# Performance work log

Measured on AMD Instinct MI355X. Metric: run time of the kernel, lower is better.

## Reference

```python
import jax, jax.numpy as jnp
import numpy as np
from jax import lax

B, T, HID, NH = 4, 2048, 1024, 16
D = HID // NH
LN_EPS = 1e-5
NORM_EPS = 1e-6


def setup_inputs() -> dict:
    key = jax.random.key(0)
    ks = jax.random.split(key, 3)
    s = 0.02
    return {
        "x": jax.random.normal(ks[0], (B, T, HID), jnp.float32),
        "ln_g": jnp.ones((HID,), jnp.float32),
        "ln_b": jnp.zeros((HID,), jnp.float32),
        "w_qkvb": jax.random.normal(ks[1], (HID, 4 * HID), jnp.float32) * s,
        "b_qkvb": jnp.zeros((4 * HID,), jnp.float32),
        "w_out": jax.random.normal(ks[2], (HID, HID), jnp.float32) * s,
        "b_out": jnp.zeros((HID,), jnp.float32),
    }


def reference(x, ln_g, ln_b, w_qkvb, b_qkvb, w_out, b_out):
    b, t = x.shape[:2]
    # LayerNorm (biased variance, eps=1e-5, matching nn.LayerNorm)
    mu = jnp.mean(x, axis=-1, keepdims=True)
    var = jnp.mean((x - mu) ** 2, axis=-1, keepdims=True)
    normed = (x - mu) * lax.rsqrt(var + LN_EPS) * ln_g + ln_b

    proj = normed @ w_qkvb + b_qkvb  # [B,T,4H]
    q, k, v, beta_pre = jnp.split(proj, 4, axis=-1)
    beta = jax.nn.sigmoid(beta_pre)

    def heads(a):  # [B,T,H] -> [T,B,NH,D] (time-major for scan)
        return a.reshape(b, t, NH, D).transpose(1, 0, 2, 3)

    q, k, v, beta = heads(q), heads(k), heads(v), heads(beta)
    # F.normalize(k, dim=-1, eps=1e-6)
    k = k / jnp.maximum(jnp.linalg.norm(k, axis=-1, keepdims=True), NORM_EPS)

    S0 = jnp.zeros((b, NH, D, D), x.dtype)

    def step(S, inp):
        q_t, k_t, v_t, beta_t = inp  # each [B,NH,D]
        retrieval = jnp.einsum('bhij,bhj->bhi', S, k_t)
        S = S + jnp.einsum('bhi,bhj->bhij', beta_t * (v_t - retrieval), k_t)
        o_t = jnp.einsum('bhij,bhj->bhi', S, q_t)
        return S, o_t

    _, out_t = lax.scan(step, S0, (q, k, v, beta))  # out_t: [T,B,NH,D]
    scan_out = out_t.transpose(1, 0, 2, 3).reshape(b, t, NH * D)
    return x + scan_out @ w_out + b_out
```

## Files before the change

### kernel.cpp

```cpp
#include <hip/hip_runtime.h>
#include <hip/hip_bf16.h>

typedef __attribute__((ext_vector_type(8))) short short8;
typedef __attribute__((ext_vector_type(4))) float f32x4;

#define P72 72

__device__ __forceinline__ unsigned short f2bf(float f) {
    union { float f; unsigned int u; } v; v.f = f;
    unsigned int r = (v.u + 0x7FFFu + ((v.u >> 16) & 1u)) >> 16;
    return (unsigned short)r;
}
__device__ __forceinline__ float bf2f(unsigned short b) {
    union { unsigned int u; float f; } v; v.u = ((unsigned int)b) << 16; return v.f;
}

#define WAVE_SYNC() do { __asm__ volatile("s_waitcnt lgkmcnt(0)" ::: "memory"); \
                         __builtin_amdgcn_sched_barrier(0); } while (0)

#define LGKM_BARRIER() do { __asm__ volatile("s_waitcnt lgkmcnt(0)" ::: "memory"); \
                            __builtin_amdgcn_s_barrier(); \
                            __builtin_amdgcn_sched_barrier(0); } while (0)

#define ASYNC16(G, L) __builtin_amdgcn_global_load_lds( \
// ... 134 lines not shown
#pragma unroll
                for (int m = 0; m < 4; m++)
#pragma unroll
                    for (int n = 0; n < 4; n++)
#pragma unroll
                        for (int j = 0; j < 4; j++) {
                            float val = acc[m][n][j] + bias_r[n];
                            if (sec == 3) val = 1.0f / (1.0f + expf(-val));
                            SMEM[(m * 16 + kg * 4 + j) * 136 + wc * 64 + n * 16 + r15] = f2bf(val);
                        }
            }
            __syncthreads();
            const int tl = tid >> 2, sg = tid & 3;
            const int gm = M0 + p * 64 + tl;
            const int b = gm >> 11, t = gm & 2047;
            const int h = hA + (sg >> 1), d0 = (sg & 1) * 32;
            const int colbase = sg * 32;
            const size_t dst = ((size_t)(b * 16 + h) * 2048 + t) * 64 + d0;
#pragma unroll
            for (int i = 0; i < 4; i++) {
                uint4 v = *(const uint4*)&SMEM[tl * 136 + colbase + i * 8];
                *(uint4*)(arr + dst + i * 8) = v;
            }
        }
    } else {
        float* stf = (float*)SMEM;
#pragma unroll
        for (int p = 0; p < 4; ++p) {
            __syncthreads();
            if (wr == (p >> 1)) {
#pragma unroll
                for (int mm = 0; mm < 2; mm++)
#pragma unroll
                    for (int n = 0; n < 4; n++)
#pragma unroll
                        for (int j = 0; j < 4; j++)
                            stf[(mm * 16 + kg * 4 + j) * 132 + wc * 64 + n * 16 + r15] =
                                acc[(p & 1) * 2 + mm][n][j] + bias_r[n];
            }
            __syncthreads();
            const int rl = tid >> 3, sg = (tid & 7) * 16;
            const size_t rowo = (size_t)(M0 + p * 32 + rl) * N + N0 + sg;
#pragma unroll
            for (int i = 0; i < 4; i++) {
                float4 v = *(const float4*)&stf[rl * 132 + sg + i * 4];
                float4 r = *(const float4*)(resid + rowo + i * 4);
                v.x += r.x; v.y += r.y; v.z += r.z; v.w += r.w;
                *(float4*)(outf + rowo + i * 4) = v;
            }
        }
    }
}

__global__ __launch_bounds__(512, 2) void gemm256(
    const unsigned short* __restrict__ A, const unsigned short* __restrict__ Bt,
    const float* __restrict__ bias, int K, int n0_off,
    unsigned short* __restrict__ qo, unsigned short* __restrict__ ko,
    unsigned short* __restrict__ vo, unsigned short* __restrict__ bo)
{
    __shared__ __align__(16) unsigned short SMEM[73728];
    const int tid = threadIdx.x;
    const int nwg = (int)(gridDim.x * gridDim.y);
    const int flat = (int)(blockIdx.y * gridDim.x + blockIdx.x);
    const int id2 = (flat & 7) * (nwg >> 3) + (flat >> 3);
    const int M0 = (id2 / (int)gridDim.x) * 256;
    const int N0 = (id2 % (int)gridDim.x) * 128 + n0_off;

    const int lane = tid & 63, wv = tid >> 6;
    const int wr = wv >> 2, wc = wv & 3;
    const int r15 = lane & 15, kg = lane >> 4;
    const int swz = r15 & 7;

    const int srow = lane >> 3;
    const int schk = (lane & 7) ^ srow;
    const unsigned short* Asrc = A  + (size_t)(M0 + wv * 8 + srow) * K + schk * 8;
    const unsigned short* Bsrc = Bt + (size_t)(N0 + wv * 8 + srow) * K + schk * 8;

    float bias_r[2];
    bias_r[0] = bias[N0 + wc * 32 + r15];
    bias_r[1] = bias[N0 + wc * 32 + 16 + r15];
    __builtin_amdgcn_sched_barrier(0);

    auto stageA = [&](int b_, int ko_, int i_) {
        ASYNC16(Asrc + (size_t)i_ * 64 * K + ko_,
                &SMEM[b_ * 24576 + (i_ * 64 + wv * 8) * 64]);
    };
    auto stageB = [&](int b_, int ko_, int i_) {
        ASYNC16(Bsrc + (size_t)i_ * 64 * K + ko_,
                &SMEM[b_ * 24576 + 16384 + (i_ * 64 + wv * 8) * 64]);
    };

#pragma unroll
    for (int i = 0; i < 4; i++) stageA(0, 0, i);
    stageB(0, 0, 0); stageB(0, 0, 1);
#pragma unroll
    for (int i = 0; i < 4; i++) stageA(1, 64, i);
    stageB(1, 64, 0); stageB(1, 64, 1);

    f32x4 acc[8][2] = {};

#define PH_PRE() do { __builtin_amdgcn_s_barrier(); \
                      __asm__ volatile("s_waitcnt lgkmcnt(0)" ::: "memory"); \
                      __builtin_amdgcn_sched_barrier(0); \
                      __builtin_amdgcn_s_setprio(1); } while (0)
#define PH_POST() do { __builtin_amdgcn_s_setprio(0); \
                       __builtin_amdgcn_sched_barrier(0); \
                       __builtin_amdgcn_s_barrier(); } while (0)

    const int NT = K >> 6;
    int cur = 0;
    for (int t = 0; t < NT; ++t) {
        if (t + 1 < NT) { __asm__ volatile("s_waitcnt vmcnt(6)" ::: "memory"); }
        else            { __asm__ volatile("s_waitcnt vmcnt(0)" ::: "memory"); }
        __builtin_amdgcn_s_barrier();
        __builtin_amdgcn_sched_barrier(0);

        const unsigned short* Ab = &SMEM[cur * 24576];
        const unsigned short* Bb = &SMEM[cur * 24576 + 16384];
        int nb = cur + 2; if (nb >= 3) nb -= 3;
        const int nko = (t + 2) * 64;
        const bool pf = (t + 2 < NT);

        short8 af[4], bf[2];
#pragma unroll
        for (int m = 0; m < 4; m++)
            af[m] = *(const short8*)&Ab[(wr * 128 + m * 16 + r15) * 64 + (kg ^ swz) * 8];
#pragma unroll
        for (int n = 0; n < 2; n++)
            bf[n] = *(const short8*)&Bb[(wc * 32 + n * 16 + r15) * 64 + (kg ^ swz) * 8];
        if (pf) { stageA(nb, nko, 0); stageA(nb, nko, 1); }
        PH_PRE();
#pragma unroll
        for (int m = 0; m < 4; m++)
#pragma unroll
            for (int n = 0; n < 2; n++)
                acc[m][n] = __builtin_amdgcn_mfma_f32_16x16x32_bf16(af[m], bf[n], acc[m][n], 0, 0, 0);
        PH_POST();
#pragma unroll
        for (int m = 0; m < 4; m++)
            af[m] = *(const short8*)&Ab[(wr * 128 + (m + 4) * 16 + r15) * 64 + (kg ^ swz) * 8];
        if (pf) { stageA(nb, nko, 2); stageA(nb, nko, 3); }
        PH_PRE();
#pragma unroll
        for (int m = 0; m < 4; m++)
#pragma unroll
            for (int n = 0; n < 2; n++)
                acc[m + 4][n] = __builtin_amdgcn_mfma_f32_16x16x32_bf16(af[m], bf[n], acc[m + 4][n], 0, 0, 0);
        PH_POST();
#pragma unroll
        for (int m = 0; m < 4; m++)
            af[m] = *(const short8*)&Ab[(wr * 128 + m * 16 + r15) * 64 + ((4 + kg) ^ swz) * 8];
#pragma unroll
        for (int n = 0; n < 2; n++)
            bf[n] = *(const short8*)&Bb[(wc * 32 + n * 16 + r15) * 64 + ((4 + kg) ^ swz) * 8];
        if (pf) { stageB(nb, nko, 0); stageB(nb, nko, 1); }
        PH_PRE();
#pragma unroll
        for (int m = 0; m < 4; m++)
#pragma unroll
            for (int n = 0; n < 2; n++)
                acc[m][n] = __builtin_amdgcn_mfma_f32_16x16x32_bf16(af[m], bf[n], acc[m][n], 0, 0, 0);
        PH_POST();
#pragma unroll
        for (int m = 0; m < 4; m++)
            af[m] = *(const short8*)&Ab[(wr * 128 + (m + 4) * 16 + r15) * 64 + ((4 + kg) ^ swz) * 8];
        PH_PRE();
#pragma unroll
        for (int m = 0; m < 4; m++)
#pragma unroll
            for (int n = 0; n < 2; n++)
                acc[m + 4][n] = __builtin_amdgcn_mfma_f32_16x16x32_bf16(af[m], bf[n], acc[m + 4][n], 0, 0, 0);
        __builtin_amdgcn_s_setprio(0);
        __builtin_amdgcn_sched_barrier(0);

        cur += 1; if (cur >= 3) cur = 0;
    }
#undef PH_PRE
#undef PH_POST

    const int sec = N0 >> 10;
    const int hA = (N0 & 1023) >> 6;
    unsigned short* arr = (sec == 0) ? qo : (sec == 1) ? ko : (sec == 2) ? vo : bo;
#pragma unroll
    for (int p = 0; p < 2; ++p) {
        __syncthreads();
        if (wr == p) {
#pragma unroll
            for (int m = 0; m < 8; m++)
#pragma unroll
                for (int n = 0; n < 2; n++)
#pragma unroll
                    for (int j = 0; j < 4; j++) {
                        float val = acc[m][n][j] + bias_r[n];
                        if (sec == 3) val = 1.0f / (1.0f + expf(-val));
                        SMEM[(m * 16 + kg * 4 + j) * 136 + wc * 32 + n * 16 + r15] = f2bf(val);
                    }
        }
        __syncthreads();
        const int row = tid >> 2, sg = tid & 3;
        const int gm = M0 + p * 128 + row;
        const int b = gm >> 11, tt = gm & 2047;
        const int h = hA + (sg >> 1), d0 = (sg & 1) * 32;
        const size_t dst = ((size_t)(b * 16 + h) * 2048 + tt) * 64 + d0;
#pragma unroll
        for (int i = 0; i < 4; i++) {
            uint4 v = *(const uint4*)&SMEM[row * 136 + sg * 32 + i * 8];
            *(uint4*)(arr + dst + i * 8) = v;
        }
    }
}

__global__ __launch_bounds__(256) void prep_kernel(
    const unsigned short* __restrict__ Kpre, const unsigned short* __restrict__ Vin,
    const unsigned short* __restrict__ Bin,
    unsigned short* __restrict__ Kb, unsigned short* __restrict__ A0g,
    float* __restrict__ A0Dg, unsigned short* __restrict__ KTg,
    unsigned short* __restrict__ VTg, unsigned short* __restrict__ BTg)
{
    __shared__ __align__(16) unsigned short Ks[64 * P72];
    __shared__ __align__(16) unsigned short Vs[64 * P72];
    __shared__ __align__(16) unsigned short Bs[64 * P72];
    __shared__ __align__(16) unsigned short Os[64 * P72];
    const int cid = blockIdx.x, tid = threadIdx.x;
    const size_t gbase = (size_t)cid * 4096;
    const int r0 = tid >> 2, c0 = (tid & 3) * 16;
    {
        uint4 k0 = *(const uint4*)(Kpre + gbase + r0 * 64 + c0), k1 = *(const uint4*)(Kpre + gbase + r0 * 64 + c0 + 8);
        uint4 v0 = *(const uint4*)(Vin + gbase + r0 * 64 + c0),  v1 = *(const uint4*)(Vin + gbase + r0 * 64 + c0 + 8);
        uint4 b0 = *(const uint4*)(Bin + gbase + r0 * 64 + c0),  b1 = *(const uint4*)(Bin + gbase + r0 * 64 + c0 + 8);
        *(uint4*)&Ks[r0 * P72 + c0] = k0; *(uint4*)&Ks[r0 * P72 + c0 + 8] = k1;
        *(uint4*)&Vs[r0 * P72 + c0] = v0; *(uint4*)&Vs[r0 * P72 + c0 + 8] = v1;
        *(uint4*)&Bs[r0 * P72 + c0] = b0; *(uint4*)&Bs[r0 * P72 + c0 + 8] = b1;
    }
    __syncthreads();
    {
        const int row = tid >> 2, seg = tid & 3;
        float v[16]; float ss = 0.f;
#pragma unroll
        for (int q = 0; q < 16; q++) { v[q] = bf2f(Ks[row * P72 + seg * 16 + q]); ss = fmaf(v[q], v[q], ss); }
        ss += __shfl_xor(ss, 1); ss += __shfl_xor(ss, 2);
        const float inv = 1.0f / fmaxf(sqrtf(ss), 1e-6f);
        unsigned short t16[16];
#pragma unroll
        for (int q = 0; q < 16; q++) t16[q] = f2bf(v[q] * inv);
        *(uint4*)&Ks[row * P72 + seg * 16]     = *(uint4*)&t16[0];
        *(uint4*)&Ks[row * P72 + seg * 16 + 8] = *(uint4*)&t16[8];
        *(uint4*)(Kb + gbase + row * 64 + seg * 16)     = *(uint4*)&t16[0];
        *(uint4*)(Kb + gbase + row * 64 + seg * 16 + 8) = *(uint4*)&t16[8];
    }
    __syncthreads();
    const int lane = tid & 63, w = tid >> 6;
    const int r15 = lane & 15, kg = lane >> 4;
    f32x4 acc[4] = {{0,0,0,0},{0,0,0,0},{0,0,0,0},{0,0,0,0}};
#pragma unroll
    for (int ks = 0; ks < 2; ks++) {
        short8 afr = *(const short8*)&Ks[(w * 16 + r15) * P72 + ks * 32 + kg * 8];
#pragma unroll
        for (int n = 0; n < 4; n++) {
            short8 bfr = *(const short8*)&Ks[(n * 16 + r15) * P72 + ks * 32 + kg * 8];
            acc[n] = __builtin_amdgcn_mfma_f32_16x16x32_bf16(afr, bfr, acc[n], 0, 0, 0);
        }
    }
#pragma unroll
    for (int n = 0; n < 4; n++) {
#pragma unroll
        for (int j = 0; j < 4; j++) {
            const int s = w * 16 + kg * 4 + j, r = n * 16 + r15;
            Os[s * P72 + r] = (r < s) ? f2bf(acc[n][j]) : (unsigned short)0;
        }
        if (n == w) {
            float4 d;
            d.x = (r15 < kg * 4 + 0) ? acc[n][0] : 0.f;
            d.y = (r15 < kg * 4 + 1) ? acc[n][1] : 0.f;
            d.z = (r15 < kg * 4 + 2) ? acc[n][2] : 0.f;
            d.w = (r15 < kg * 4 + 3) ? acc[n][3] : 0.f;
            *(float4*)(A0Dg + (size_t)cid * 1024 + w * 256 + r15 * 16 + kg * 4) = d;
        }
    }
    __syncthreads();
    {
        uint4 x0 = *(const uint4*)&Os[r0 * P72 + c0];
        uint4 x1 = *(const uint4*)&Os[r0 * P72 + c0 + 8];
        *(uint4*)(A0g + gbase + r0 * 64 + c0) = x0;
        *(uint4*)(A0g + gbase + r0 * 64 + c0 + 8) = x1;
    }
    {
        const int d = tid >> 2, s0 = (tid & 3) * 16;
        unsigned short tk[16], tv[16], tb[16];
#pragma unroll
        for (int k = 0; k < 16; k++) {
            tk[k] = Ks[(s0 + k) * P72 + d];
            tv[k] = Vs[(s0 + k) * P72 + d];
            tb[k] = Bs[(s0 + k) * P72 + d];
        }
        *(uint4*)(KTg + gbase + (size_t)d * 64 + s0)     = *(uint4*)&tk[0];
        *(uint4*)(KTg + gbase + (size_t)d * 64 + s0 + 8) = *(uint4*)&tk[8];
        *(uint4*)(VTg + gbase + (size_t)d * 64 + s0)     = *(uint4*)&tv[0];
        *(uint4*)(VTg + gbase + (size_t)d * 64 + s0 + 8) = *(uint4*)&tv[8];
        *(uint4*)(BTg + gbase + (size_t)d * 64 + s0)     = *(uint4*)&tb[0];
        *(uint4*)(BTg + gbase + (size_t)d * 64 + s0 + 8) = *(uint4*)&tb[8];
    }
}

__global__ __launch_bounds__(256, 1) void fused_scan_kernel(
    const unsigned short* __restrict__ A0g, const unsigned short* __restrict__ Kb,
    const unsigned short* __restrict__ KTg, const float* __restrict__ A0Dg,
    const unsigned short* __restrict__ VTg, const unsigned short* __restrict__ BTg,
    unsigned short* __restrict__ Scg, unsigned short* __restrict__ UTg,
    const unsigned short* __restrict__ NORM, const unsigned short* __restrict__ WQT,
    const float* __restrict__ bias, unsigned short* __restrict__ qo,
    const float* __restrict__ w_out, unsigned short* __restrict__ WOT)
{
    __shared__ __align__(16) unsigned char POOL[120832];
    unsigned short* us = (unsigned short*)POOL;
    const int tid = threadIdx.x;

    if (blockIdx.x < 64) {
        unsigned short* sK  = us;
        unsigned short* sKT = us + 9216;
        unsigned short* sA0 = us + 18432;
        unsigned short* sVT = us + 27648;
        unsigned short* sBT = us + 36864;
        float* sA0D = (float*)(POOL + 92160);
        unsigned short* Sbf = us + 51200;
        unsigned short* UTs = us + 55808;

        const int bh = blockIdx.x;
        const int lane = tid & 63, w = tid >> 6;
        const int r15 = lane & 15, kg = lane >> 4;
        const int sr = tid >> 2, sc = (tid & 3) * 16;
        const int qr = 16 * w + (lane >> 2), qc = (lane & 3) * 16;
        const size_t base0 = (size_t)bh * 32 * 4096;
        const size_t baseD = (size_t)bh * 32 * 1024;
        const int dOff = (w * 16 + (sr & 15)) * 20 + (tid & 3) * 4;

        f32x4 Sreg[4] = {};
        uint4 g[10]; float4 gD;

        const uint4 z4 = {0u, 0u, 0u, 0u};
        *(uint4*)&Sbf[sr * P72 + sc] = z4;
        *(uint4*)&Sbf[sr * P72 + sc + 8] = z4;
        {
            const size_t gb = base0 + sr * 64 + sc;
            g[0] = *(const uint4*)(Kb  + gb); g[1] = *(const uint4*)(Kb  + gb + 8);
            g[2] = *(const uint4*)(KTg + gb); g[3] = *(const uint4*)(KTg + gb + 8);
            g[4] = *(const uint4*)(A0g + gb); g[5] = *(const uint4*)(A0g + gb + 8);
            g[6] = *(const uint4*)(VTg + gb); g[7] = *(const uint4*)(VTg + gb + 8);
            g[8] = *(const uint4*)(BTg + gb); g[9] = *(const uint4*)(BTg + gb + 8);
            gD   = *(const float4*)(A0Dg + baseD + tid * 4);
            *(uint4*)&sK [sr * P72 + sc] = g[0]; *(uint4*)&sK [sr * P72 + sc + 8] = g[1];
            *(uint4*)&sKT[sr * P72 + sc] = g[2]; *(uint4*)&sKT[sr * P72 + sc + 8] = g[3];
            *(uint4*)&sA0[sr * P72 + sc] = g[4]; *(uint4*)&sA0[sr * P72 + sc + 8] = g[5];
            *(uint4*)&sVT[sr * P72 + sc] = g[6]; *(uint4*)&sVT[sr * P72 + sc + 8] = g[7];
            *(uint4*)&sBT[sr * P72 + sc] = g[8]; *(uint4*)&sBT[sr * P72 + sc + 8] = g[9];
            *(float4*)&sA0D[dOff] = gD;
        }

#pragma unroll 1
        for (int c = 0; c < 32; ++c) {
            const int cur = c & 1, nxt = cur ^ 1;
            LGKM_BARRIER();
            if (c < 31) {
                const size_t gb = base0 + (size_t)(c + 1) * 4096 + sr * 64 + sc;
                g[0] = *(const uint4*)(Kb  + gb); g[1] = *(const uint4*)(Kb  + gb + 8);
                g[2] = *(const uint4*)(KTg + gb); g[3] = *(const uint4*)(KTg + gb + 8);
                g[4] = *(const uint4*)(A0g + gb); g[5] = *(const uint4*)(A0g + gb + 8);
                g[6] = *(const uint4*)(VTg + gb); g[7] = *(const uint4*)(VTg + gb + 8);
                g[8] = *(const uint4*)(BTg + gb); g[9] = *(const uint4*)(BTg + gb + 8);
                gD   = *(const float4*)(A0Dg + baseD + (size_t)(c + 1) * 1024 + tid * 4);
            }
            const unsigned short* KsC  = &sK [cur * 4608];
            const unsigned short* KTsC = &sKT[cur * 4608];
            const unsigned short* A0C  = &sA0[cur * 4608];
            const unsigned short* VTC  = &sVT[cur * 4608];
            const unsigned short* BTC  = &sBT[cur * 4608];
            const float*          A0DC = &sA0D[cur * 1280];

            *(uint4*)&UTs[(16 * w + r15) * P72 + kg * 16] = z4;
            *(uint4*)&UTs[(16 * w + r15) * P72 + kg * 16 + 8] = z4;

            {
                uint4 a = *(const uint4*)&Sbf[qr * P72 + qc];
                uint4 b2 = *(const uint4*)&Sbf[qr * P72 + qc + 8];
                const unsigned FL = 0x80008000u;
                a.x ^= FL; a.y ^= FL; a.z ^= FL; a.w ^= FL;
                b2.x ^= FL; b2.y ^= FL; b2.z ^= FL; b2.w ^= FL;
                const size_t so = base0 + (size_t)c * 4096 + qr * 64 + qc;
                *(uint4*)(Scg + so) = a;
                *(uint4*)(Scg + so + 8) = b2;
            }

            f32x4 y[4];
#pragma unroll
            for (int st = 0; st < 4; st++) {
                ushort4 vv = *(const ushort4*)&VTC[(16 * w + r15) * P72 + st * 16 + kg * 4];
                y[st][0] = bf2f(vv.x); y[st][1] = bf2f(vv.y);
                y[st][2] = bf2f(vv.z); y[st][3] = bf2f(vv.w);
            }
#pragma unroll
            for (int ks = 0; ks < 2; ks++) {
                short8 bfr = *(const short8*)&Sbf[(16 * w + r15) * P72 + ks * 32 + kg * 8];
#pragma unroll
                for (int st = 0; st < 4; st++) {
                    short8 afr = *(const short8*)&KsC[(st * 16 + r15) * P72 + ks * 32 + kg * 8];
                    y[st] = __builtin_amdgcn_mfma_f32_16x16x32_bf16(afr, bfr, y[st], 0, 0, 0);
                }
            }

#pragma unroll
            for (int b = 0; b < 4; b++) {
                if (b > 0) {
                    WAVE_SYNC();
                    f32x4 corr = {};
                    {
                        short8 afr = *(const short8*)&A0C[(b * 16 + r15) * P72 + kg * 8];
                        short8 bfr = *(const short8*)&UTs[(16 * w + r15) * P72 + kg * 8];
                        corr = __builtin_amdgcn_mfma_f32_16x16x32_bf16(afr, bfr, corr, 0, 0, 0);
                    }
                    if (b == 3) {
                        short8 afr = *(const short8*)&A0C[(b * 16 + r15) * P72 + 32 + kg * 8];
                        short8 bfr = *(const short8*)&UTs[(16 * w + r15) * P72 + 32 + kg * 8];
                        corr = __builtin_amdgcn_mfma_f32_16x16x32_bf16(afr, bfr, corr, 0, 0, 0);
                    }
                    y[b] = y[b] - corr;
                }
                ushort4 bt4 = *(const ushort4*)&BTC[(16 * w + r15) * P72 + b * 16 + kg * 4];
                const float bta0 = bf2f(bt4.x), bta1 = bf2f(bt4.y);
                const float bta2 = bf2f(bt4.z), bta3 = bf2f(bt4.w);
                float us0 = 0.f, us1 = 0.f, us2 = 0.f, us3 = 0.f;
#pragma unroll
                for (int own = 0; own < 4; own++) {
                    const f32x4 c40 = *(const f32x4*)&A0DC[(b * 16 + own * 4 + 0) * 20 + kg * 4];
                    const f32x4 c41 = *(const f32x4*)&A0DC[(b * 16 + own * 4 + 1) * 20 + kg * 4];
                    const f32x4 c42 = *(const f32x4*)&A0DC[(b * 16 + own * 4 + 2) * 20 + kg * 4];
                    const f32x4 c43 = *(const f32x4*)&A0DC[(b * 16 + own * 4 + 3) * 20 + kg * 4];
                    if (kg == own) {
                        us0 = bta0 * y[b][0];
                        us1 = bta1 * (y[b][1] - c40[1] * us0);
                        us2 = bta2 * (y[b][2] - c40[2] * us0 - c41[2] * us1);
                        us3 = bta3 * (y[b][3] - c40[3] * us0 - c41[3] * us1 - c42[3] * us2);
                    }
                    const int src = own * 16 + r15;
                    const float u0 = __shfl(us0, src), u1 = __shfl(us1, src);
                    const float u2 = __shfl(us2, src), u3 = __shfl(us3, src);
                    if (kg > own)
                        y[b] = y[b] - (c40 * u0 + c41 * u1 + c42 * u2 + c43 * u3);
                }
                ushort4 up;
                up.x = f2bf(us0); up.y = f2bf(us1); up.z = f2bf(us2); up.w = f2bf(us3);
                *(ushort4*)&UTs[(16 * w + r15) * P72 + b * 16 + kg * 4] = up;
            }
            WAVE_SYNC();

            {
                uint4 a = *(const uint4*)&UTs[qr * P72 + qc];
                uint4 b2 = *(const uint4*)&UTs[qr * P72 + qc + 8];
                const size_t so = base0 + (size_t)c * 4096 + qr * 64 + qc;
                *(uint4*)(UTg + so) = a;
                *(uint4*)(UTg + so + 8) = b2;
            }

#pragma unroll
            for (int ks = 0; ks < 2; ks++) {
                short8 afr = *(const short8*)&UTs[(16 * w + r15) * P72 + ks * 32 + kg * 8];
#pragma unroll
                for (int n = 0; n < 4; n++) {
                    short8 bfr = *(const short8*)&KTsC[(n * 16 + r15) * P72 + ks * 32 + kg * 8];
                    Sreg[n] = __builtin_amdgcn_mfma_f32_16x16x32_bf16(afr, bfr, Sreg[n], 0, 0, 0);
                }
            }
#pragma unroll
            for (int n = 0; n < 4; n++)
#pragma unroll
                for (int jj = 0; jj < 4; jj++)
                    Sbf[(16 * w + kg * 4 + jj) * P72 + n * 16 + r15] = f2bf(-Sreg[n][jj]);

            if (c < 31) {
                *(uint4*)&sK [nxt * 4608 + sr * P72 + sc] = g[0]; *(uint4*)&sK [nxt * 4608 + sr * P72 + sc + 8] = g[1];
                *(uint4*)&sKT[nxt * 4608 + sr * P72 + sc] = g[2]; *(uint4*)&sKT[nxt * 4608 + sr * P72 + sc + 8] = g[3];
                *(uint4*)&sA0[nxt * 4608 + sr * P72 + sc] = g[4]; *(uint4*)&sA0[nxt * 4608 + sr * P72 + sc + 8] = g[5];
                *(uint4*)&sVT[nxt * 4608 + sr * P72 + sc] = g[6]; *(uint4*)&sVT[nxt * 4608 + sr * P72 + sc + 8] = g[7];
                *(uint4*)&sBT[nxt * 4608 + sr * P72 + sc] = g[8]; *(uint4*)&sBT[nxt * 4608 + sr * P72 + sc + 8] = g[9];
                *(float4*)&sA0D[nxt * 1280 + dOff] = gD;
            }
        }
    } else if (blockIdx.x < 64 + 512) {
        unsigned short* SMEM = us;
        const int blk = blockIdx.x - 64;
        const int M0 = (blk >> 3) * 128, N0 = (blk & 7) * 128;
        const int K = 1024;
        const int lane = tid & 63;
        const int w = tid >> 6, wr = w >> 1, wc = w & 1;
        const int r15 = lane & 15, kg = lane >> 4;
        const int lr = lane >> 2, lc = (lane & 3) * 8;

        const unsigned short* Arow0 = NORM + (size_t)(M0 + w * 16 + lr) * K + lc;
        const unsigned short* Arow1 = NORM + (size_t)(M0 + 64 + w * 16 + lr) * K + lc;
        const unsigned short* Brow0 = WQT + (size_t)(N0 + w * 16 + lr) * K + lc;
        const unsigned short* Brow1 = WQT + (size_t)(N0 + 64 + w * 16 + lr) * K + lc;

        f32x4 acc[4][4] = {};

        ASYNC16(Arow0, &SMEM[(w * 16) * 32]);
        ASYNC16(Arow1, &SMEM[(64 + w * 16) * 32]);
        ASYNC16(Brow0, &SMEM[8192 + (w * 16) * 32]);
        ASYNC16(Brow1, &SMEM[8192 + (64 + w * 16) * 32]);

        int cur = 0;
        for (int k0 = 0; k0 < K; k0 += 32) {
            if (k0 + 32 < K) {
                const int nb = (cur ^ 1) * 4096;
                ASYNC16(Arow0 + k0 + 32, &SMEM[nb + (w * 16) * 32]);
                ASYNC16(Arow1 + k0 + 32, &SMEM[nb + (64 + w * 16) * 32]);
                ASYNC16(Brow0 + k0 + 32, &SMEM[8192 + nb + (w * 16) * 32]);
                ASYNC16(Brow1 + k0 + 32, &SMEM[8192 + nb + (64 + w * 16) * 32]);
                __asm__ volatile("s_waitcnt vmcnt(4)" ::: "memory");
            } else {
                __asm__ volatile("s_waitcnt vmcnt(0)" ::: "memory");
            }
            __builtin_amdgcn_s_barrier();
            __builtin_amdgcn_sched_barrier(0);
            const int cb = cur * 4096;
            short8 af[4], bf[4];
#pragma unroll
            for (int m = 0; m < 4; m++)
                af[m] = *(const short8*)&SMEM[cb + (wr * 64 + m * 16 + r15) * 32 + kg * 8];
#pragma unroll
            for (int n = 0; n < 4; n++)
                bf[n] = *(const short8*)&SMEM[8192 + cb + (wc * 64 + n * 16 + r15) * 32 + kg * 8];
#pragma unroll
            for (int m = 0; m < 4; m++)
#pragma unroll
                for (int n = 0; n < 4; n++)
                    acc[m][n] = __builtin_amdgcn_mfma_f32_16x16x32_bf16(af[m], bf[n], acc[m][n], 0, 0, 0);
            __builtin_amdgcn_sched_barrier(0);
            __builtin_amdgcn_s_barrier();
            cur ^= 1;
        }

        float bias_r[4];
#pragma unroll
        for (int n = 0; n < 4; n++) bias_r[n] = bias[N0 + wc * 64 + n * 16 + r15];
        const int hA = N0 >> 6;
#pragma unroll
        for (int p = 0; p < 2; ++p) {
            __syncthreads();
            if (wr == p) {
#pragma unroll
                for (int m = 0; m < 4; m++)
#pragma unroll
                    for (int n = 0; n < 4; n++)
#pragma unroll
                        for (int j = 0; j < 4; j++)
                            SMEM[(m * 16 + kg * 4 + j) * 136 + wc * 64 + n * 16 + r15] =
                                f2bf(acc[m][n][j] + bias_r[n]);
            }
            __syncthreads();
            const int tl = tid >> 2, sg = tid & 3;
            const int gm = M0 + p * 64 + tl;
            const int b = gm >> 11, t = gm & 2047;
            const int h = hA + (sg >> 1), d0 = (sg & 1) * 32;
            const int colbase = sg * 32;
            const size_t dst = ((size_t)(b * 16 + h) * 2048 + t) * 64 + d0;
#pragma unroll
            for (int i = 0; i < 4; i++) {
                uint4 v = *(const uint4*)&SMEM[tl * 136 + colbase + i * 8];
                *(uint4*)(qo + dst + i * 8) = v;
            }
        }
    } else {
        float* tile = (float*)POOL;
        const int blk = blockIdx.x - 64 - 512;
        const int c0 = (blk & 31) * 32, r0 = (blk >> 5) * 32;
        const int tx = tid & 31, ty = tid >> 5;
#pragma unroll
        for (int yy = 0; yy < 32; yy += 8)
            tile[(ty + yy) * 33 + tx] = w_out[(size_t)(r0 + ty + yy) * 1024 + c0 + tx];
        __syncthreads();
#pragma unroll
        for (int yy = 0; yy < 32; yy += 8)
            WOT[(size_t)(c0 + ty + yy) * 1024 + r0 + tx] = f2bf(tile[tx * 33 + ty + yy]);
    }
}

__global__ __launch_bounds__(256) void out_kernel(
    const unsigned short* __restrict__ Qb, const unsigned short* __restrict__ Kb,
    const unsigned short* __restrict__ Scg, const unsigned short* __restrict__ UTg,
    unsigned short* __restrict__ attn)
{
    __shared__ __align__(16) unsigned short Qs[64 * P72];
    __shared__ __align__(16) unsigned short Kbs[64 * P72];
    __shared__ __align__(16) unsigned short Scs[64 * P72];
    __shared__ __align__(16) unsigned short UTss[64 * P72];
    __shared__ __align__(16) unsigned short Ms[64 * P72];
    __shared__ __align__(16) unsigned short Osb[64 * P72];
    const int blk = blockIdx.x, tid = threadIdx.x;
    const int bh = blk >> 5, cc = blk & 31;
    const size_t gbase = (size_t)blk * 4096;
    const int lane = tid & 63, w = tid >> 6;
    const int r15 = lane & 15, kg = lane >> 4;
    {
        const int r0 = tid >> 2, c0 = (tid & 3) * 16;
        uint4 q0 = *(const uint4*)(Qb + gbase + r0 * 64 + c0),  q1 = *(const uint4*)(Qb + gbase + r0 * 64 + c0 + 8);
        uint4 k0 = *(const uint4*)(Kb + gbase + r0 * 64 + c0),  k1 = *(const uint4*)(Kb + gbase + r0 * 64 + c0 + 8);
        uint4 s0 = *(const uint4*)(Scg + gbase + r0 * 64 + c0), s1 = *(const uint4*)(Scg + gbase + r0 * 64 + c0 + 8);
        uint4 u0 = *(const uint4*)(UTg + gbase + r0 * 64 + c0), u1 = *(const uint4*)(UTg + gbase + r0 * 64 + c0 + 8);
        *(uint4*)&Qs [r0 * P72 + c0] = q0; *(uint4*)&Qs [r0 * P72 + c0 + 8] = q1;
        *(uint4*)&Kbs[r0 * P72 + c0] = k0; *(uint4*)&Kbs[r0 * P72 + c0 + 8] = k1;
        *(uint4*)&Scs[r0 * P72 + c0] = s0; *(uint4*)&Scs[r0 * P72 + c0 + 8] = s1;
        *(uint4*)&UTss[r0 * P72 + c0] = u0; *(uint4*)&UTss[r0 * P72 + c0 + 8] = u1;
    }
    __syncthreads();
    {
        f32x4 accm[4] = {{0,0,0,0},{0,0,0,0},{0,0,0,0},{0,0,0,0}};
#pragma unroll
        for (int ks = 0; ks < 2; ks++) {
            short8 afr = *(const short8*)&Qs[(w * 16 + r15) * P72 + ks * 32 + kg * 8];
#pragma unroll
            for (int n = 0; n < 4; n++) {
                short8 bfr = *(const short8*)&Kbs[(n * 16 + r15) * P72 + ks * 32 + kg * 8];
                accm[n] = __builtin_amdgcn_mfma_f32_16x16x32_bf16(afr, bfr, accm[n], 0, 0, 0);
            }
        }
#pragma unroll
        for (int n = 0; n < 4; n++)
#pragma unroll
            for (int j = 0; j < 4; j++) {
                const int t = w * 16 + kg * 4 + j, s = n * 16 + r15;
                Ms[t * P72 + s] = (s <= t) ? f2bf(accm[n][j]) : (unsigned short)0;
            }
    }
    __syncthreads();
    {
        f32x4 acc[4] = {{0,0,0,0},{0,0,0,0},{0,0,0,0},{0,0,0,0}};
#pragma unroll
        for (int ks = 0; ks < 2; ks++) {
            short8 afr = *(const short8*)&Qs[(w * 16 + r15) * P72 + ks * 32 + kg * 8];
#pragma unroll
            for (int n = 0; n < 4; n++) {
                short8 bfr = *(const short8*)&Scs[(n * 16 + r15) * P72 + ks * 32 + kg * 8];
                acc[n] = __builtin_amdgcn_mfma_f32_16x16x32_bf16(afr, bfr, acc[n], 0, 0, 0);
            }
        }
#pragma unroll
        for (int ks = 0; ks < 2; ks++) {
            short8 afr = *(const short8*)&Ms[(w * 16 + r15) * P72 + ks * 32 + kg * 8];
#pragma unroll
            for (int n = 0; n < 4; n++) {
                short8 bfr = *(const short8*)&UTss[(n * 16 + r15) * P72 + ks * 32 + kg * 8];
                acc[n] = __builtin_amdgcn_mfma_f32_16x16x32_bf16(afr, bfr, acc[n], 0, 0, 0);
            }
        }
#pragma unroll
        for (int n = 0; n < 4; n++)
#pragma unroll
            for (int j = 0; j < 4; j++) {
                const int t = w * 16 + kg * 4 + j, i = n * 16 + r15;
                Osb[t * P72 + i] = f2bf(acc[n][j]);
            }
    }
    __syncthreads();
    {
        const int b = bh >> 4, h = bh & 15;
        const int t = tid >> 2, i0 = (tid & 3) * 16;
        uint4 o0 = *(const uint4*)&Osb[t * P72 + i0];
        uint4 o1 = *(const uint4*)&Osb[t * P72 + i0 + 8];
        unsigned short* dst = attn + ((size_t)(b * 2048 + cc * 64 + t)) * 1024 + h * 64 + i0;
        *(uint4*)dst = o0;
        *(uint4*)(dst + 8) = o1;
    }
}

extern "C" void kernel_launch(void* const* d_in, const int* in_sizes, int n_in,
                              void* d_out, int out_size, void* d_ws, size_t ws_size,
                              hipStream_t stream)
{
    const float* x      = (const float*)d_in[0];
    const float* ln_g   = (const float*)d_in[1];
    const float* ln_b   = (const float*)d_in[2];
    const float* w_qkvb = (const float*)d_in[3];
    const float* b_qkvb = (const float*)d_in[4];
    const float* w_out  = (const float*)d_in[5];
    const float* b_out  = (const float*)d_in[6];
    float* out = (float*)d_out;

    char* ws = (char*)d_ws;
    size_t off = 0;
    auto alloc = [&](size_t bytes) -> char* {
        char* p = ws + off;
        off = (off + bytes + 255) & ~(size_t)255;
        return p;
    };
    const size_t TOK = 64ull * 2048 * 64;
    unsigned short* WQT  = (unsigned short*)alloc(4096ull * 1024 * 2);
    unsigned short* WOT  = (unsigned short*)alloc(1024ull * 1024 * 2);
    unsigned short* NORM = (unsigned short*)alloc(TOK * 2 * 2);
    unsigned short* Qb   = (unsigned short*)alloc(TOK * 2);
    unsigned short* Kpre = (unsigned short*)alloc(TOK * 2);
    unsigned short* Kb   = (unsigned short*)alloc(TOK * 2);
    unsigned short* KTb  = (unsigned short*)alloc(TOK * 2);
    unsigned short* Vb   = (unsigned short*)alloc(TOK * 2);
    unsigned short* Bb   = (unsigned short*)alloc(TOK * 2);
    unsigned short* A0   = (unsigned short*)alloc(TOK * 2);
    unsigned short* Sc   = (unsigned short*)alloc(TOK * 2);
    unsigned short* UT   = (unsigned short*)alloc(TOK * 2);
    float*          A0D  = (float*)alloc(2048ull * 1024 * 4);
    unsigned short* ATTN = NORM;
    unsigned short* VTb  = Vb;
    unsigned short* BTb  = Bb;

    hipLaunchKernelGGL(ln_wqt_kernel, dim3(8192 + 4096), dim3(256), 0, stream,
                       x, ln_g, ln_b, NORM, w_qkvb, WQT);
    hipLaunchKernelGGL(gemm256, dim3(24, 32), dim3(512), 0, stream,
                       NORM, WQT, b_qkvb, 1024, 1024, Qb, Kpre, Vb, Bb);
    hipLaunchKernelGGL(prep_kernel, dim3(2048), dim3(256), 0, stream,
                       Kpre, Vb, Bb, Kb, A0, A0D, KTb, VTb, BTb);
    hipLaunchKernelGGL(fused_scan_kernel, dim3(64 + 512 + 1024), dim3(256), 0, stream,
                       A0, Kb, KTb, A0D, VTb, BTb, Sc, UT,
                       NORM, WQT, b_qkvb, Qb, w_out, WOT);
    hipLaunchKernelGGL(out_kernel, dim3(2048), dim3(256), 0, stream, Qb, Kb, Sc, UT, ATTN);
    hipLaunchKernelGGL(gemm128, dim3(8, 64), dim3(256), 0, stream,
                       ATTN, WOT, b_out, 1024, 1024, 1, 0,
                       x, out, (unsigned short*)nullptr, (unsigned short*)nullptr,
                       (unsigned short*)nullptr, (unsigned short*)nullptr);
}
```

Baseline: 330.3 us.

## Pack two scan heads per 512-thread block with single-buffered LDS staging

Each fused_scan block now runs 512 threads and handles two independent heads, each with its own LDS region. The GEMM and weight-transpose roles are likewise packed two tiles per block, and the grid is halved. The LDS double buffering for the next chunk is replaced by a single buffer guarded by extra block-wide barriers. The goal is to fit more per-head work on each CU and free CUs for the other roles, at the cost of extra barrier stalls and two scans competing for one CU's matrix units.

```diff
diff --git a/kernel.cpp b/kernel.cpp
--- a/kernel.cpp
+++ b/kernel.cpp
@@ -460,7 +460,7 @@
     }
 }
 
-__global__ __launch_bounds__(256, 1) void fused_scan_kernel(
+__global__ __launch_bounds__(512, 1) void fused_scan_kernel(
     const unsigned short* __restrict__ A0g, const unsigned short* __restrict__ Kb,
     const unsigned short* __restrict__ KTg, const float* __restrict__ A0Dg,
     const unsigned short* __restrict__ VTg, const unsigned short* __restrict__ BTg,
@@ -469,28 +469,31 @@
     const float* __restrict__ bias, unsigned short* __restrict__ qo,
     const float* __restrict__ w_out, unsigned short* __restrict__ WOT)
 {
-    __shared__ __align__(16) unsigned char POOL[120832];
+    __shared__ __align__(16) unsigned char POOL[139264];
     unsigned short* us = (unsigned short*)POOL;
     const int tid = threadIdx.x;
 
-    if (blockIdx.x < 64) {
-        unsigned short* sK  = us;
-        unsigned short* sKT = us + 9216;
-        unsigned short* sA0 = us + 18432;
-        unsigned short* sVT = us + 27648;
-        unsigned short* sBT = us + 36864;
-        float* sA0D = (float*)(POOL + 92160);
-        unsigned short* Sbf = us + 51200;
-        unsigned short* UTs = us + 55808;
-
-        const int bh = blockIdx.x;
-        const int lane = tid & 63, w = tid >> 6;
+    if (blockIdx.x < 32) {
+        const int grp = tid >> 8;
+        const int tl  = tid & 255;
+        const int bh  = blockIdx.x * 2 + grp;
+        unsigned short* usG = us + grp * 34816;
+        unsigned short* sK  = usG;
+        unsigned short* sKT = usG + 4608;
+        unsigned short* sA0 = usG + 9216;
+        unsigned short* sVT = usG + 13824;
+        unsigned short* sBT = usG + 18432;
+        unsigned short* Sbf = usG + 23040;
+        unsigned short* UTs = usG + 27648;
+        float* sA0D = (float*)(POOL + grp * 69632 + 64512);
+
+        const int lane = tl & 63, w = tl >> 6;
         const int r15 = lane & 15, kg = lane >> 4;
-        const int sr = tid >> 2, sc = (tid & 3) * 16;
+        const int sr = tl >> 2, sc = (tl & 3) * 16;
         const int qr = 16 * w + (lane >> 2), qc = (lane & 3) * 16;
         const size_t base0 = (size_t)bh * 32 * 4096;
         const size_t baseD = (size_t)bh * 32 * 1024;
-        const int dOff = (w * 16 + (sr & 15)) * 20 + (tid & 3) * 4;
+        const int dOff = (w * 16 + (sr & 15)) * 20 + (tl & 3) * 4;
 
         f32x4 Sreg[4] = {};
         uint4 g[10]; float4 gD;
@@ -505,7 +508,7 @@
             g[4] = *(const uint4*)(A0g + gb); g[5] = *(const uint4*)(A0g + gb + 8);
             g[6] = *(const uint4*)(VTg + gb); g[7] = *(const uint4*)(VTg + gb + 8);
             g[8] = *(const uint4*)(BTg + gb); g[9] = *(const uint4*)(BTg + gb + 8);
-            gD   = *(const float4*)(A0Dg + baseD + tid * 4);
+            gD   = *(const float4*)(A0Dg + baseD + tl * 4);
             *(uint4*)&sK [sr * P72 + sc] = g[0]; *(uint4*)&sK [sr * P72 + sc + 8] = g[1];
             *(uint4*)&sKT[sr * P72 + sc] = g[2]; *(uint4*)&sKT[sr * P72 + sc + 8] = g[3];
             *(uint4*)&sA0[sr * P72 + sc] = g[4]; *(uint4*)&sA0[sr * P72 + sc + 8] = g[5];
@@ -513,11 +516,10 @@
             *(uint4*)&sBT[sr * P72 + sc] = g[8]; *(uint4*)&sBT[sr * P72 + sc + 8] = g[9];
             *(float4*)&sA0D[dOff] = gD;
         }
+        LGKM_BARRIER();
 
 #pragma unroll 1
         for (int c = 0; c < 32; ++c) {
-            const int cur = c & 1, nxt = cur ^ 1;
-            LGKM_BARRIER();
             if (c < 31) {
                 const size_t gb = base0 + (size_t)(c + 1) * 4096 + sr * 64 + sc;
                 g[0] = *(const uint4*)(Kb  + gb); g[1] = *(const uint4*)(Kb  + gb + 8);
@@ -525,14 +527,8 @@
                 g[4] = *(const uint4*)(A0g + gb); g[5] = *(const uint4*)(A0g + gb + 8);
                 g[6] = *(const uint4*)(VTg + gb); g[7] = *(const uint4*)(VTg + gb + 8);
                 g[8] = *(const uint4*)(BTg + gb); g[9] = *(const uint4*)(BTg + gb + 8);
-                gD   = *(const float4*)(A0Dg + baseD + (size_t)(c + 1) * 1024 + tid * 4);
-            }
-            const unsigned short* KsC  = &sK [cur * 4608];
-            const unsigned short* KTsC = &sKT[cur * 4608];
-            const unsigned short* A0C  = &sA0[cur * 4608];
-            const unsigned short* VTC  = &sVT[cur * 4608];
-            const unsigned short* BTC  = &sBT[cur * 4608];
-            const float*          A0DC = &sA0D[cur * 1280];
+                gD   = *(const float4*)(A0Dg + baseD + (size_t)(c + 1) * 1024 + tl * 4);
+            }
 
             *(uint4*)&UTs[(16 * w + r15) * P72 + kg * 16] = z4;
             *(uint4*)&UTs[(16 * w + r15) * P72 + kg * 16 + 8] = z4;
@@ -551,7 +547,7 @@
             f32x4 y[4];
 #pragma unroll
             for (int st = 0; st < 4; st++) {
-                ushort4 vv = *(const ushort4*)&VTC[(16 * w + r15) * P72 + st * 16 + kg * 4];
+                ushort4 vv = *(const ushort4*)&sVT[(16 * w + r15) * P72 + st * 16 + kg * 4];
                 y[st][0] = bf2f(vv.x); y[st][1] = bf2f(vv.y);
                 y[st][2] = bf2f(vv.z); y[st][3] = bf2f(vv.w);
             }
@@ -560,7 +556,7 @@
                 short8 bfr = *(const short8*)&Sbf[(16 * w + r15) * P72 + ks * 32 + kg * 8];
 #pragma unroll
                 for (int st = 0; st < 4; st++) {
-                    short8 afr = *(const short8*)&KsC[(st * 16 + r15) * P72 + ks * 32 + kg * 8];
+                    short8 afr = *(const short8*)&sK[(st * 16 + r15) * P72 + ks * 32 + kg * 8];
                     y[st] = __builtin_amdgcn_mfma_f32_16x16x32_bf16(afr, bfr, y[st], 0, 0, 0);
                 }
             }
@@ -571,27 +567,27 @@
                     WAVE_SYNC();
                     f32x4 corr = {};
                     {
-                        short8 afr = *(const short8*)&A0C[(b * 16 + r15) * P72 + kg * 8];
+                        short8 afr = *(const short8*)&sA0[(b * 16 + r15) * P72 + kg * 8];
                         short8 bfr = *(const short8*)&UTs[(16 * w + r15) * P72 + kg * 8];
                         corr = __builtin_amdgcn_mfma_f32_16x16x32_bf16(afr, bfr, corr, 0, 0, 0);
                     }
                     if (b == 3) {
-                        short8 afr = *(const short8*)&A0C[(b * 16 + r15) * P72 + 32 + kg * 8];
+                        short8 afr = *(const short8*)&sA0[(b * 16 + r15) * P72 + 32 + kg * 8];
                         short8 bfr = *(const short8*)&UTs[(16 * w + r15) * P72 + 32 + kg * 8];
                         corr = __builtin_amdgcn_mfma_f32_16x16x32_bf16(afr, bfr, corr, 0, 0, 0);
                     }
                     y[b] = y[b] - corr;
                 }
-                ushort4 bt4 = *(const ushort4*)&BTC[(16 * w + r15) * P72 + b * 16 + kg * 4];
+                ushort4 bt4 = *(const ushort4*)&sBT[(16 * w + r15) * P72 + b * 16 + kg * 4];
                 const float bta0 = bf2f(bt4.x), bta1 = bf2f(bt4.y);
                 const float bta2 = bf2f(bt4.z), bta3 = bf2f(bt4.w);
                 float us0 = 0.f, us1 = 0.f, us2 = 0.f, us3 = 0.f;
 #pragma unroll
                 for (int own = 0; own < 4; own++) {
-                    const f32x4 c40 = *(const f32x4*)&A0DC[(b * 16 + own * 4 + 0) * 20 + kg * 4];
-                    const f32x4 c41 = *(const f32x4*)&A0DC[(b * 16 + own * 4 + 1) * 20 + kg * 4];
-                    const f32x4 c42 = *(const f32x4*)&A0DC[(b * 16 + own * 4 + 2) * 20 + kg * 4];
-                    const f32x4 c43 = *(const f32x4*)&A0DC[(b * 16 + own * 4 + 3) * 20 + kg * 4];
+                    const f32x4 c40 = *(const f32x4*)&sA0D[(b * 16 + own * 4 + 0) * 20 + kg * 4];
+                    const f32x4 c41 = *(const f32x4*)&sA0D[(b * 16 + own * 4 + 1) * 20 + kg * 4];
+                    const f32x4 c42 = *(const f32x4*)&sA0D[(b * 16 + own * 4 + 2) * 20 + kg * 4];
+                    const f32x4 c43 = *(const f32x4*)&sA0D[(b * 16 + own * 4 + 3) * 20 + kg * 4];
                     if (kg == own) {
                         us0 = bta0 * y[b][0];
                         us1 = bta1 * (y[b][1] - c40[1] * us0);
@@ -623,7 +619,7 @@
                 short8 afr = *(const short8*)&UTs[(16 * w + r15) * P72 + ks * 32 + kg * 8];
 #pragma unroll
                 for (int n = 0; n < 4; n++) {
-                    short8 bfr = *(const short8*)&KTsC[(n * 16 + r15) * P72 + ks * 32 + kg * 8];
+                    short8 bfr = *(const short8*)&sKT[(n * 16 + r15) * P72 + ks * 32 + kg * 8];
                     Sreg[n] = __builtin_amdgcn_mfma_f32_16x16x32_bf16(afr, bfr, Sreg[n], 0, 0, 0);
                 }
             }
@@ -633,22 +629,26 @@
                 for (int jj = 0; jj < 4; jj++)
                     Sbf[(16 * w + kg * 4 + jj) * P72 + n * 16 + r15] = f2bf(-Sreg[n][jj]);
 
+            LGKM_BARRIER();
             if (c < 31) {
-                *(uint4*)&sK [nxt * 4608 + sr * P72 + sc] = g[0]; *(uint4*)&sK [nxt * 4608 + sr * P72 + sc + 8] = g[1];
-                *(uint4*)&sKT[nxt * 4608 + sr * P72 + sc] = g[2]; *(uint4*)&sKT[nxt * 4608 + sr * P72 + sc + 8] = g[3];
-                *(uint4*)&sA0[nxt * 4608 + sr * P72 + sc] = g[4]; *(uint4*)&sA0[nxt * 4608 + sr * P72 + sc + 8] = g[5];
-                *(uint4*)&sVT[nxt * 4608 + sr * P72 + sc] = g[6]; *(uint4*)&sVT[nxt * 4608 + sr * P72 + sc + 8] = g[7];
-                *(uint4*)&sBT[nxt * 4608 + sr * P72 + sc] = g[8]; *(uint4*)&sBT[nxt * 4608 + sr * P72 + sc + 8] = g[9];
-                *(float4*)&sA0D[nxt * 1280 + dOff] = gD;
-            }
-        }
-    } else if (blockIdx.x < 64 + 512) {
-        unsigned short* SMEM = us;
-        const int blk = blockIdx.x - 64;
-        const int M0 = (blk >> 3) * 128, N0 = (blk & 7) * 128;
+                *(uint4*)&sK [sr * P72 + sc] = g[0]; *(uint4*)&sK [sr * P72 + sc + 8] = g[1];
+                *(uint4*)&sKT[sr * P72 + sc] = g[2]; *(uint4*)&sKT[sr * P72 + sc + 8] = g[3];
+                *(uint4*)&sA0[sr * P72 + sc] = g[4]; *(uint4*)&sA0[sr * P72 + sc + 8] = g[5];
+                *(uint4*)&sVT[sr * P72 + sc] = g[6]; *(uint4*)&sVT[sr * P72 + sc + 8] = g[7];
+                *(uint4*)&sBT[sr * P72 + sc] = g[8]; *(uint4*)&sBT[sr * P72 + sc + 8] = g[9];
+                *(float4*)&sA0D[dOff] = gD;
+                LGKM_BARRIER();
+            }
+        }
+    } else if (blockIdx.x < 32 + 256) {
+        const int half = tid >> 8, tl = tid & 255;
+        unsigned short* SMEM = us + half * 18432;
+        const int raw = blockIdx.x - 32;
+        const int M0 = (raw >> 2) * 128;
+        const int N0 = ((raw & 3) * 2 + half) * 128;
         const int K = 1024;
-        const int lane = tid & 63;
-        const int w = tid >> 6, wr = w >> 1, wc = w & 1;
+        const int lane = tl & 63;
+        const int w = tl >> 6, wr = w >> 1, wc = w & 1;
         const int r15 = lane & 15, kg = lane >> 4;
         const int lr = lane >> 2, lc = (lane & 3) * 8;
 
@@ -714,23 +714,24 @@
                                 f2bf(acc[m][n][j] + bias_r[n]);
             }
             __syncthreads();
-            const int tl = tid >> 2, sg = tid & 3;
-            const int gm = M0 + p * 64 + tl;
+            const int tl2 = tl >> 2, sg = tl & 3;
+            const int gm = M0 + p * 64 + tl2;
             const int b = gm >> 11, t = gm & 2047;
             const int h = hA + (sg >> 1), d0 = (sg & 1) * 32;
             const int colbase = sg * 32;
             const size_t dst = ((size_t)(b * 16 + h) * 2048 + t) * 64 + d0;
 #pragma unroll
             for (int i = 0; i < 4; i++) {
-                uint4 v = *(const uint4*)&SMEM[tl * 136 + colbase + i * 8];
+                uint4 v = *(const uint4*)&SMEM[tl2 * 136 + colbase + i * 8];
                 *(uint4*)(qo + dst + i * 8) = v;
             }
         }
     } else {
-        float* tile = (float*)POOL;
-        const int blk = blockIdx.x - 64 - 512;
+        const int half = tid >> 8, tl = tid & 255;
+        float* tile = (float*)POOL + half * 1056;
+        const int blk = (blockIdx.x - 32 - 256) * 2 + half;
         const int c0 = (blk & 31) * 32, r0 = (blk >> 5) * 32;
-        const int tx = tid & 31, ty = tid >> 5;
+        const int tx = tl & 31, ty = tl >> 5;
 #pragma unroll
         for (int yy = 0; yy < 32; yy += 8)
             tile[(ty + yy) * 33 + tx] = w_out[(size_t)(r0 + ty + yy) * 1024 + c0 + tx];
@@ -873,7 +874,7 @@
                        NORM, WQT, b_qkvb, 1024, 1024, Qb, Kpre, Vb, Bb);
     hipLaunchKernelGGL(prep_kernel, dim3(2048), dim3(256), 0, stream,
                        Kpre, Vb, Bb, Kb, A0, A0D, KTb, VTb, BTb);
-    hipLaunchKernelGGL(fused_scan_kernel, dim3(64 + 512 + 1024), dim3(256), 0, stream,
+    hipLaunchKernelGGL(fused_scan_kernel, dim3(32 + 256 + 512), dim3(512), 0, stream,
                        A0, Kb, KTb, A0D, VTb, BTb, Sc, UT,
                        NORM, WQT, b_qkvb, Qb, w_out, WOT);
     hipLaunchKernelGGL(out_kernel, dim3(2048), dim3(256), 0, stream, Qb, Kb, Sc, UT, ATTN);
```

Result: slower. 464.6 us (+40.7%).

## Single-buffer scan LDS to fit two blocks per CU and remap GEMM tiles

Applied to the files above, without the earlier changes.

Removes the double buffering of the per-chunk K/KT/A0/VT/BT/A0D staging in LDS, shrinking the shared pool so two blocks can be resident per CU (launch bounds raised to 2). Barriers move so that LDS writes for the next chunk happen after a barrier that follows compute, adding an extra sync per chunk. GEMM block indices are also permuted to change tile ordering across the grid. The added occupancy lets the GEMM blocks co-reside with the serial scan blocks, but the scan loses overlap between staging and compute and may face register pressure under the tighter launch bound.

```diff
diff --git a/kernel.cpp b/kernel.cpp
--- a/kernel.cpp
+++ b/kernel.cpp
@@ -460,7 +460,7 @@
     }
 }
 
-__global__ __launch_bounds__(256, 1) void fused_scan_kernel(
+__global__ __launch_bounds__(256, 2) void fused_scan_kernel(
     const unsigned short* __restrict__ A0g, const unsigned short* __restrict__ Kb,
     const unsigned short* __restrict__ KTg, const float* __restrict__ A0Dg,
     const unsigned short* __restrict__ VTg, const unsigned short* __restrict__ BTg,
@@ -469,19 +469,19 @@
     const float* __restrict__ bias, unsigned short* __restrict__ qo,
     const float* __restrict__ w_out, unsigned short* __restrict__ WOT)
 {
-    __shared__ __align__(16) unsigned char POOL[120832];
+    __shared__ __align__(16) unsigned char POOL[69632];
     unsigned short* us = (unsigned short*)POOL;
     const int tid = threadIdx.x;
 
     if (blockIdx.x < 64) {
         unsigned short* sK  = us;
-        unsigned short* sKT = us + 9216;
-        unsigned short* sA0 = us + 18432;
-        unsigned short* sVT = us + 27648;
-        unsigned short* sBT = us + 36864;
-        float* sA0D = (float*)(POOL + 92160);
-        unsigned short* Sbf = us + 51200;
-        unsigned short* UTs = us + 55808;
+        unsigned short* sKT = us + 4608;
+        unsigned short* sA0 = us + 9216;
+        unsigned short* sVT = us + 13824;
+        unsigned short* sBT = us + 18432;
+        unsigned short* Sbf = us + 23040;
+        unsigned short* UTs = us + 27648;
+        float* sA0D = (float*)(POOL + 64512);
 
         const int bh = blockIdx.x;
         const int lane = tid & 63, w = tid >> 6;
@@ -513,11 +513,10 @@
             *(uint4*)&sBT[sr * P72 + sc] = g[8]; *(uint4*)&sBT[sr * P72 + sc + 8] = g[9];
             *(float4*)&sA0D[dOff] = gD;
         }
+        LGKM_BARRIER();
 
 #pragma unroll 1
         for (int c = 0; c < 32; ++c) {
-            const int cur = c & 1, nxt = cur ^ 1;
-            LGKM_BARRIER();
             if (c < 31) {
                 const size_t gb = base0 + (size_t)(c + 1) * 4096 + sr * 64 + sc;
                 g[0] = *(const uint4*)(Kb  + gb); g[1] = *(const uint4*)(Kb  + gb + 8);
@@ -527,12 +526,6 @@
                 g[8] = *(const uint4*)(BTg + gb); g[9] = *(const uint4*)(BTg + gb + 8);
                 gD   = *(const float4*)(A0Dg + baseD + (size_t)(c + 1) * 1024 + tid * 4);
             }
-            const unsigned short* KsC  = &sK [cur * 4608];
-            const unsigned short* KTsC = &sKT[cur * 4608];
-            const unsigned short* A0C  = &sA0[cur * 4608];
-            const unsigned short* VTC  = &sVT[cur * 4608];
-            const unsigned short* BTC  = &sBT[cur * 4608];
-            const float*          A0DC = &sA0D[cur * 1280];
 
             *(uint4*)&UTs[(16 * w + r15) * P72 + kg * 16] = z4;
             *(uint4*)&UTs[(16 * w + r15) * P72 + kg * 16 + 8] = z4;
@@ -551,7 +544,7 @@
             f32x4 y[4];
 #pragma unroll
             for (int st = 0; st < 4; st++) {
-                ushort4 vv = *(const ushort4*)&VTC[(16 * w + r15) * P72 + st * 16 + kg * 4];
+                ushort4 vv = *(const ushort4*)&sVT[(16 * w + r15) * P72 + st * 16 + kg * 4];
                 y[st][0] = bf2f(vv.x); y[st][1] = bf2f(vv.y);
                 y[st][2] = bf2f(vv.z); y[st][3] = bf2f(vv.w);
             }
@@ -560,7 +553,7 @@
                 short8 bfr = *(const short8*)&Sbf[(16 * w + r15) * P72 + ks * 32 + kg * 8];
 #pragma unroll
                 for (int st = 0; st < 4; st++) {
-                    short8 afr = *(const short8*)&KsC[(st * 16 + r15) * P72 + ks * 32 + kg * 8];
+                    short8 afr = *(const short8*)&sK[(st * 16 + r15) * P72 + ks * 32 + kg * 8];
                     y[st] = __builtin_amdgcn_mfma_f32_16x16x32_bf16(afr, bfr, y[st], 0, 0, 0);
                 }
             }
@@ -571,27 +564,27 @@
                     WAVE_SYNC();
                     f32x4 corr = {};
                     {
-                        short8 afr = *(const short8*)&A0C[(b * 16 + r15) * P72 + kg * 8];
+                        short8 afr = *(const short8*)&sA0[(b * 16 + r15) * P72 + kg * 8];
                         short8 bfr = *(const short8*)&UTs[(16 * w + r15) * P72 + kg * 8];
                         corr = __builtin_amdgcn_mfma_f32_16x16x32_bf16(afr, bfr, corr, 0, 0, 0);
                     }
                     if (b == 3) {
-                        short8 afr = *(const short8*)&A0C[(b * 16 + r15) * P72 + 32 + kg * 8];
+                        short8 afr = *(const short8*)&sA0[(b * 16 + r15) * P72 + 32 + kg * 8];
                         short8 bfr = *(const short8*)&UTs[(16 * w + r15) * P72 + 32 + kg * 8];
                         corr = __builtin_amdgcn_mfma_f32_16x16x32_bf16(afr, bfr, corr, 0, 0, 0);
                     }
                     y[b] = y[b] - corr;
                 }
-                ushort4 bt4 = *(const ushort4*)&BTC[(16 * w + r15) * P72 + b * 16 + kg * 4];
+                ushort4 bt4 = *(const ushort4*)&sBT[(16 * w + r15) * P72 + b * 16 + kg * 4];
                 const float bta0 = bf2f(bt4.x), bta1 = bf2f(bt4.y);
                 const float bta2 = bf2f(bt4.z), bta3 = bf2f(bt4.w);
                 float us0 = 0.f, us1 = 0.f, us2 = 0.f, us3 = 0.f;
 #pragma unroll
                 for (int own = 0; own < 4; own++) {
-                    const f32x4 c40 = *(const f32x4*)&A0DC[(b * 16 + own * 4 + 0) * 20 + kg * 4];
-                    const f32x4 c41 = *(const f32x4*)&A0DC[(b * 16 + own * 4 + 1) * 20 + kg * 4];
-                    const f32x4 c42 = *(const f32x4*)&A0DC[(b * 16 + own * 4 + 2) * 20 + kg * 4];
-                    const f32x4 c43 = *(const f32x4*)&A0DC[(b * 16 + own * 4 + 3) * 20 + kg * 4];
+                    const f32x4 c40 = *(const f32x4*)&sA0D[(b * 16 + own * 4 + 0) * 20 + kg * 4];
+                    const f32x4 c41 = *(const f32x4*)&sA0D[(b * 16 + own * 4 + 1) * 20 + kg * 4];
+                    const f32x4 c42 = *(const f32x4*)&sA0D[(b * 16 + own * 4 + 2) * 20 + kg * 4];
+                    const f32x4 c43 = *(const f32x4*)&sA0D[(b * 16 + own * 4 + 3) * 20 + kg * 4];
                     if (kg == own) {
                         us0 = bta0 * y[b][0];
                         us1 = bta1 * (y[b][1] - c40[1] * us0);
@@ -623,7 +616,7 @@
                 short8 afr = *(const short8*)&UTs[(16 * w + r15) * P72 + ks * 32 + kg * 8];
 #pragma unroll
                 for (int n = 0; n < 4; n++) {
-                    short8 bfr = *(const short8*)&KTsC[(n * 16 + r15) * P72 + ks * 32 + kg * 8];
+                    short8 bfr = *(const short8*)&sKT[(n * 16 + r15) * P72 + ks * 32 + kg * 8];
                     Sreg[n] = __builtin_amdgcn_mfma_f32_16x16x32_bf16(afr, bfr, Sreg[n], 0, 0, 0);
                 }
             }
@@ -633,19 +626,22 @@
                 for (int jj = 0; jj < 4; jj++)
                     Sbf[(16 * w + kg * 4 + jj) * P72 + n * 16 + r15] = f2bf(-Sreg[n][jj]);
 
+            LGKM_BARRIER();
             if (c < 31) {
-                *(uint4*)&sK [nxt * 4608 + sr * P72 + sc] = g[0]; *(uint4*)&sK [nxt * 4608 + sr * P72 + sc + 8] = g[1];
-                *(uint4*)&sKT[nxt * 4608 + sr * P72 + sc] = g[2]; *(uint4*)&sKT[nxt * 4608 + sr * P72 + sc + 8] = g[3];
-                *(uint4*)&sA0[nxt * 4608 + sr * P72 + sc] = g[4]; *(uint4*)&sA0[nxt * 4608 + sr * P72 + sc + 8] = g[5];
-                *(uint4*)&sVT[nxt * 4608 + sr * P72 + sc] = g[6]; *(uint4*)&sVT[nxt * 4608 + sr * P72 + sc + 8] = g[7];
-                *(uint4*)&sBT[nxt * 4608 + sr * P72 + sc] = g[8]; *(uint4*)&sBT[nxt * 4608 + sr * P72 + sc + 8] = g[9];
-                *(float4*)&sA0D[nxt * 1280 + dOff] = gD;
+                *(uint4*)&sK [sr * P72 + sc] = g[0]; *(uint4*)&sK [sr * P72 + sc + 8] = g[1];
+                *(uint4*)&sKT[sr * P72 + sc] = g[2]; *(uint4*)&sKT[sr * P72 + sc + 8] = g[3];
+                *(uint4*)&sA0[sr * P72 + sc] = g[4]; *(uint4*)&sA0[sr * P72 + sc + 8] = g[5];
+                *(uint4*)&sVT[sr * P72 + sc] = g[6]; *(uint4*)&sVT[sr * P72 + sc + 8] = g[7];
+                *(uint4*)&sBT[sr * P72 + sc] = g[8]; *(uint4*)&sBT[sr * P72 + sc + 8] = g[9];
+                *(float4*)&sA0D[dOff] = gD;
+                LGKM_BARRIER();
             }
         }
     } else if (blockIdx.x < 64 + 512) {
         unsigned short* SMEM = us;
         const int blk = blockIdx.x - 64;
-        const int M0 = (blk >> 3) * 128, N0 = (blk & 7) * 128;
+        const int id2 = (blk & 7) * 64 + (blk >> 3);
+        const int M0 = (id2 >> 3) * 128, N0 = (id2 & 7) * 128;
         const int K = 1024;
         const int lane = tid & 63;
         const int w = tid >> 6, wr = w >> 1, wc = w & 1;
```

Measured after the change: 367.9 us. +11.4%, slower.
